# Kernel optimization log

Measured on AMD Instinct MI355X. Metric: run time of the kernel, lower is better.

Reference implementation:

```python
import jax, jax.numpy as jnp
import numpy as np

B, H, I = 4096, 128, 128


def setup_inputs() -> dict:
    key = jax.random.key(0)
    ks = jax.random.split(key, 9)
    # xavier_uniform for W1/W2: fan_in = 2H*2I, fan_out = H*2I (torch treats dim0 as fan_out for >2D differently,
    # but we only need a plausible init; exact init values don't affect correctness of the math)
    def xavier(k, shape):
        fan_in = shape[1] * shape[2] if len(shape) == 3 else shape[0]
        fan_out = shape[0] * shape[2] if len(shape) == 3 else shape[1]
        lim = np.sqrt(6.0 / (fan_in + fan_out))
        return jax.random.uniform(k, shape, jnp.float32, -lim, lim)
    W1 = xavier(ks[0], (H, 2 * H, 2 * I))
    W2 = xavier(ks[1], (H, 2 * H, 2 * I))
    W3 = xavier(ks[2], (2 * H, H))
    fan_in, fan_out = 2 * H * 2 * I, H * 2 * I
    lim = float(np.sqrt(3.0 / (0.5 * (fan_in + fan_out))))
    b1 = jax.random.uniform(ks[3], (H,), jnp.float32, -lim, lim)
    b2 = jax.random.uniform(ks[4], (H,), jnp.float32, -lim, lim)
    in0 = jax.random.normal(ks[5], (B, I), jnp.float32)
    in1 = jax.random.normal(ks[6], (B, I), jnp.float32)
    st0 = jax.random.normal(ks[7], (B, H), jnp.float32)
    st1 = jax.random.normal(ks[8], (B, H), jnp.float32)
    return {"in0": in0, "in1": in1, "st0": st0, "st1": st1,
            "W1": W1, "b1": b1, "W2": W2, "b2": b2, "W3": W3}


def reference(in0, in1, st0, st1, W1, b1, W2, b2, W3):
    s = jnp.concatenate([st0, st1], axis=1)  # [B, 2H]
    x = jnp.concatenate([in0, in1], axis=1)  # [B, 2I]
    # Trilinear contraction; same math as outer-product-then-contract:
    # einsum('ij,ik->ijk') then ('ijk,ljk->il')  ==  'bj,bk,ljk->bl'
    m1 = jnp.einsum('bj,bk,ljk->bl', s, x, W1)  # [B, H]
    m2 = jnp.einsum('bj,bk,ljk->bl', s, x, W2)  # [B, H]
    u = jax.nn.sigmoid(m2 + b2)
    state_tilda = jnp.tanh(m1 + b1)
    new_state = u * state_tilda + (1.0 - u) * (s @ W3)
    return new_state
```

## Files before the change

kernel.cpp:

```cpp
#include <hip/hip_runtime.h>
#include <hip/hip_bf16.h>
#include <stdint.h>


typedef short bf8 __attribute__((ext_vector_type(8)));
typedef float f32x4 __attribute__((ext_vector_type(4)));

static constexpr size_t WT_OFF  = 0;
static constexpr size_t XBF_OFF = 33554432 + 2097152;
static constexpr size_t MP_OFF  = XBF_OFF + 2097152;

__device__ __forceinline__ unsigned f2bf(float f) {
    unsigned u = __builtin_bit_cast(unsigned, f);
    return (u + 0x7fffu + ((u >> 16) & 1u)) >> 16;
}
__device__ __forceinline__ unsigned pack2bf(float a, float b) {
    return f2bf(a) | (f2bf(b) << 16);
}

__global__ void prep_w(const float* __restrict__ W1, const float* __restrict__ W2,
                       unsigned* __restrict__ Wt) {
    unsigned u = blockIdx.x * 256 + threadIdx.x;
    size_t e = (size_t)u * 8;
    unsigned n = (unsigned)(e >> 16);
    unsigned k = (unsigned)(e & 65535u);
    const float* src = (n < 128 ? W1 + ((size_t)n << 16)
                                : W2 + ((size_t)(n - 128) << 16)) + k;
    float4 a = ((const float4*)src)[0];
    float4 b = ((const float4*)src)[1];
    uint4 o;
    o.x = pack2bf(a.x, a.y); o.y = pack2bf(a.z, a.w);
    o.z = pack2bf(b.x, b.y); o.w = pack2bf(b.z, b.w);
    ((uint4*)Wt)[u] = o;
}

__global__ void prep_x(const float* __restrict__ in0, const float* __restrict__ in1,
                       unsigned* __restrict__ x_bf) {
    unsigned v = blockIdx.x * 256 + threadIdx.x;
    unsigned b = v >> 6;
    unsigned j4 = (v & 63u) * 4u;
    const float* src = (j4 < 128) ? (in0 + (size_t)b * 128 + j4)
                                  : (in1 + (size_t)b * 128 + (j4 - 128));
    float4 a = *(const float4*)src;
    uint2 o;
    o.x = pack2bf(a.x, a.y);
    o.y = pack2bf(a.z, a.w);
    ((uint2*)x_bf)[v] = o;
}

__launch_bounds__(256, 2)
__global__ void gemm_p(const __hip_bfloat16* __restrict__ Wt,
                       const float* __restrict__ st0, const float* __restrict__ st1,
                       const __hip_bfloat16* __restrict__ x_bf,
                       float* __restrict__ Mpart) {
    const int bx = blockIdx.x;
    const int mt = bx & 31;
    const int nt = (bx >> 5) & 1;
    const int ks = bx >> 6;
    const int b0 = mt << 7, n0 = nt << 7;
    const int tid  = threadIdx.x;
    const int lane = tid & 63, wave = tid >> 6;
    const int l15 = lane & 15, l4 = lane >> 4;

    __shared__ __align__(16) unsigned char Wl[16384];
    __shared__ __align__(16) float Sl[32 * 132];

    for (int idx = tid; idx < 4096; idx += 256) {
        int r = idx >> 5, j = idx & 31;
        int jg = ks * 32 + j;
        float v = (jg < 128) ? st0[(size_t)(b0 + r) * 128 + jg]
                             : st1[(size_t)(b0 + r) * 128 + (jg - 128)];
        Sl[j * 132 + r] = v;
    }

    const __hip_bfloat16* wgp[4];
    unsigned char* wlp[4];
    #pragma unroll
    for (int i = 0; i < 4; ++i) {
        int slot = (wave * 4 + i) * 64 + lane;
        int r = slot >> 3;
        int g = (slot & 7) ^ (r & 7);
        wgp[i] = Wt + (((size_t)(n0 + r)) << 16) + g * 8;
        wlp[i] = Wl + (wave * 4 + i) * 1024;
    }

    const unsigned char* pB = Wl + (wave * 32 + l15) * 128;
    const int be = lane & 7;
    const float* sB = Sl + l4 * 4;

    f32x4 racc[8][2];
    #pragma unroll
    for (int mf = 0; mf < 8; ++mf)
        #pragma unroll
        for (int nf = 0; nf < 2; ++nf)
            racc[mf][nf] = (f32x4){0.f, 0.f, 0.f, 0.f};

    const f32x4 zacc = (f32x4){0.f, 0.f, 0.f, 0.f};

    __syncthreads();

    for (int q = 0; q < 4; ++q) {
        bf8 a[8][2];
        const __hip_bfloat16* xb = x_bf + q * 64 + l4 * 8;
        #pragma unroll
        for (int mf = 0; mf < 8; ++mf)
            #pragma unroll
            for (int kst = 0; kst < 2; ++kst)
                a[mf][kst] = *(const bf8*)(xb + (size_t)(b0 + mf * 16 + l15) * 256 + kst * 32);

        for (int j = 0; j < 32; ++j) {
            const int koff = (ks * 32 + j) * 256 + q * 64;
            #pragma unroll
            for (int i = 0; i < 4; ++i) {
                __builtin_amdgcn_global_load_lds(
                    (__attribute__((address_space(1))) const unsigned*)(const void*)(wgp[i] + koff),
                    (__attribute__((address_space(3))) unsigned*)(void*)wlp[i],
                    16, 0, 0);
            }
            __syncthreads();

            f32x4 sv[8];
            #pragma unroll
            for (int mf = 0; mf < 8; ++mf)
                sv[mf] = *(const f32x4*)(sB + j * 132 + mf * 16);

            #pragma unroll
            for (int nf = 0; nf < 2; ++nf) {
                const unsigned char* pBn = pB + nf * 2048;
                bf8 bf0 = *(const bf8*)(pBn + ((0 + l4) ^ be) * 16);
                bf8 bf1 = *(const bf8*)(pBn + ((4 + l4) ^ be) * 16);
                #pragma unroll
                for (int mf = 0; mf < 8; ++mf) {
                    f32x4 m0 = __builtin_amdgcn_mfma_f32_16x16x32_bf16(a[mf][0], bf0, zacc, 0, 0, 0);
                    m0 = __builtin_amdgcn_mfma_f32_16x16x32_bf16(a[mf][1], bf1, m0, 0, 0, 0);
                    racc[mf][nf] += sv[mf] * m0;
                }
            }
            __syncthreads();
        }
    }

    float* mp = Mpart + ((size_t)ks << 20);
    #pragma unroll
    for (int mf = 0; mf < 8; ++mf)
        #pragma unroll
        for (int nf = 0; nf < 2; ++nf) {
            int b = b0 + mf * 16 + l4 * 4;
            int n = n0 + wave * 32 + nf * 16 + l15;
            #pragma unroll
            for (int r = 0; r < 4; ++r)
                mp[(size_t)(b + r) * 256 + n] = racc[mf][nf][r];
        }
}

__global__ void epilogue(const float* __restrict__ st0, const float* __restrict__ st1,
                         const float* __restrict__ b1, const float* __restrict__ b2,
                         const float* __restrict__ W3, const float* __restrict__ Mpart,
                         float* __restrict__ out) {
    const int tid = threadIdx.x;
    const int h = tid & 127, rg = tid >> 7;
    const int bbase = blockIdx.x * 8;
    __shared__ float srow[8][256];
    #pragma unroll
    for (int i = 0; i < 8; ++i) {
        int idx = i * 256 + tid;
        int r = idx >> 8, j = idx & 255;
        float v = (j < 128) ? st0[(size_t)(bbase + r) * 128 + j]
                            : st1[(size_t)(bbase + r) * 128 + (j - 128)];
        srow[r][j] = v;
    }
    __syncthreads();
    float acc0 = 0.f, acc1 = 0.f, acc2 = 0.f, acc3 = 0.f;
    for (int j = 0; j < 256; ++j) {
        float w = W3[j * 128 + h];
        acc0 += srow[rg][j] * w;
        acc1 += srow[rg + 2][j] * w;
        acc2 += srow[rg + 4][j] * w;
        acc3 += srow[rg + 6][j] * w;
    }
    float accs[4] = {acc0, acc1, acc2, acc3};
    float bb1 = b1[h], bb2 = b2[h];
    #pragma unroll
    for (int i = 0; i < 4; ++i) {
        int b = bbase + rg + i * 2;
        float m1 = 0.f, m2 = 0.f;
        #pragma unroll
        for (int k = 0; k < 8; ++k) {
            m1 += Mpart[((size_t)k << 20) + (size_t)b * 256 + h];
            m2 += Mpart[((size_t)k << 20) + (size_t)b * 256 + 128 + h];
        }
        float u = 1.0f / (1.0f + expf(-(m2 + bb2)));
        float t = tanhf(m1 + bb1);
        out[(size_t)b * 128 + h] = u * t + (1.0f - u) * accs[i];
    }
}

extern "C" void kernel_launch(void* const* d_in, const int* in_sizes, int n_in,
                              void* d_out, int out_size, void* d_ws, size_t ws_size,
                              hipStream_t stream) {
    const float* in0 = (const float*)d_in[0];
    const float* in1 = (const float*)d_in[1];
    const float* st0 = (const float*)d_in[2];
    const float* st1 = (const float*)d_in[3];
    const float* W1  = (const float*)d_in[4];
    const float* b1  = (const float*)d_in[5];
    const float* W2  = (const float*)d_in[6];
    const float* b2  = (const float*)d_in[7];
    const float* W3  = (const float*)d_in[8];
    float* out = (float*)d_out;
    char* ws = (char*)d_ws;

    __hip_bfloat16* Wt   = (__hip_bfloat16*)(ws + WT_OFF);
    unsigned*       x_bf = (unsigned*)(ws + XBF_OFF);
    float*          Mp   = (float*)(ws + MP_OFF);

    prep_w<<<8192, 256, 0, stream>>>(W1, W2, (unsigned*)Wt);
    prep_x<<<1024, 256, 0, stream>>>(in0, in1, x_bf);
    gemm_p<<<512, 256, 0, stream>>>(Wt, st0, st1, (const __hip_bfloat16*)x_bf, Mp);
    epilogue<<<512, 256, 0, stream>>>(st0, st1, b1, b2, W3, Mp, out);
}
```

Baseline: 294.1 us.

## Load weights directly to registers with double buffering, fuse prep kernels, remap blocks

Replaces the LDS staging of bf16 weight tiles (global_load_lds plus two barriers per step) with per-lane direct global loads into registers, double-buffered one step ahead. The K-split index becomes the fastest-varying block index, so blocks sharing weight slices run concurrently and share L2. The two prep kernels are merged into one launch, and partial-sum stores become nontemporal. Each wave now loads its own weight fragments uncoalesced from global memory and holds more registers live, which may lower occupancy.

```diff
diff --git a/kernel.cpp b/kernel.cpp
--- a/kernel.cpp
+++ b/kernel.cpp
@@ -18,34 +18,35 @@
     return f2bf(a) | (f2bf(b) << 16);
 }
 
-__global__ void prep_w(const float* __restrict__ W1, const float* __restrict__ W2,
-                       unsigned* __restrict__ Wt) {
-    unsigned u = blockIdx.x * 256 + threadIdx.x;
-    size_t e = (size_t)u * 8;
-    unsigned n = (unsigned)(e >> 16);
-    unsigned k = (unsigned)(e & 65535u);
-    const float* src = (n < 128 ? W1 + ((size_t)n << 16)
-                                : W2 + ((size_t)(n - 128) << 16)) + k;
-    float4 a = ((const float4*)src)[0];
-    float4 b = ((const float4*)src)[1];
-    uint4 o;
-    o.x = pack2bf(a.x, a.y); o.y = pack2bf(a.z, a.w);
-    o.z = pack2bf(b.x, b.y); o.w = pack2bf(b.z, b.w);
-    ((uint4*)Wt)[u] = o;
-}
-
-__global__ void prep_x(const float* __restrict__ in0, const float* __restrict__ in1,
-                       unsigned* __restrict__ x_bf) {
-    unsigned v = blockIdx.x * 256 + threadIdx.x;
-    unsigned b = v >> 6;
-    unsigned j4 = (v & 63u) * 4u;
-    const float* src = (j4 < 128) ? (in0 + (size_t)b * 128 + j4)
-                                  : (in1 + (size_t)b * 128 + (j4 - 128));
-    float4 a = *(const float4*)src;
-    uint2 o;
-    o.x = pack2bf(a.x, a.y);
-    o.y = pack2bf(a.z, a.w);
-    ((uint2*)x_bf)[v] = o;
+__global__ void prep_wx(const float* __restrict__ W1, const float* __restrict__ W2,
+                        const float* __restrict__ in0, const float* __restrict__ in1,
+                        unsigned* __restrict__ Wt, unsigned* __restrict__ x_bf) {
+    int bx = blockIdx.x;
+    if (bx < 8192) {
+        unsigned u = bx * 256 + threadIdx.x;
+        size_t e = (size_t)u * 8;
+        unsigned n = (unsigned)(e >> 16);
+        unsigned k = (unsigned)(e & 65535u);
+        const float* src = (n < 128 ? W1 + ((size_t)n << 16)
+                                    : W2 + ((size_t)(n - 128) << 16)) + k;
+        float4 a = ((const float4*)src)[0];
+        float4 b = ((const float4*)src)[1];
+        uint4 o;
+        o.x = pack2bf(a.x, a.y); o.y = pack2bf(a.z, a.w);
+        o.z = pack2bf(b.x, b.y); o.w = pack2bf(b.z, b.w);
+        ((uint4*)Wt)[u] = o;
+    } else {
+        unsigned v = (bx - 8192) * 256 + threadIdx.x;
+        unsigned b = v >> 6;
+        unsigned j4 = (v & 63u) * 4u;
+        const float* src = (j4 < 128) ? (in0 + (size_t)b * 128 + j4)
+                                      : (in1 + (size_t)b * 128 + (j4 - 128));
+        float4 a = *(const float4*)src;
+        uint2 o;
+        o.x = pack2bf(a.x, a.y);
+        o.y = pack2bf(a.z, a.w);
+        ((uint2*)x_bf)[v] = o;
+    }
 }
 
 __launch_bounds__(256, 2)
@@ -54,17 +55,15 @@
                        const __hip_bfloat16* __restrict__ x_bf,
                        float* __restrict__ Mpart) {
     const int bx = blockIdx.x;
-    const int mt = bx & 31;
-    const int nt = (bx >> 5) & 1;
-    const int ks = bx >> 6;
+    const int ks = bx & 7;
+    const int nt = (bx >> 3) & 1;
+    const int mt = bx >> 4;
     const int b0 = mt << 7, n0 = nt << 7;
     const int tid  = threadIdx.x;
     const int lane = tid & 63, wave = tid >> 6;
     const int l15 = lane & 15, l4 = lane >> 4;
 
-    __shared__ __align__(16) unsigned char Wl[16384];
     __shared__ __align__(16) float Sl[32 * 132];
-
     for (int idx = tid; idx < 4096; idx += 256) {
         int r = idx >> 5, j = idx & 31;
         int jg = ks * 32 + j;
@@ -72,20 +71,9 @@
                              : st1[(size_t)(b0 + r) * 128 + (jg - 128)];
         Sl[j * 132 + r] = v;
     }
-
-    const __hip_bfloat16* wgp[4];
-    unsigned char* wlp[4];
-    #pragma unroll
-    for (int i = 0; i < 4; ++i) {
-        int slot = (wave * 4 + i) * 64 + lane;
-        int r = slot >> 3;
-        int g = (slot & 7) ^ (r & 7);
-        wgp[i] = Wt + (((size_t)(n0 + r)) << 16) + g * 8;
-        wlp[i] = Wl + (wave * 4 + i) * 1024;
-    }
-
-    const unsigned char* pB = Wl + (wave * 32 + l15) * 128;
-    const int be = lane & 7;
+    __syncthreads();
+
+    const __hip_bfloat16* rb = Wt + ((size_t)(n0 + wave * 32 + l15) << 16) + l4 * 8;
     const float* sB = Sl + l4 * 4;
 
     f32x4 racc[8][2];
@@ -94,49 +82,54 @@
         #pragma unroll
         for (int nf = 0; nf < 2; ++nf)
             racc[mf][nf] = (f32x4){0.f, 0.f, 0.f, 0.f};
-
     const f32x4 zacc = (f32x4){0.f, 0.f, 0.f, 0.f};
 
-    __syncthreads();
-
-    for (int q = 0; q < 4; ++q) {
-        bf8 a[8][2];
-        const __hip_bfloat16* xb = x_bf + q * 64 + l4 * 8;
+    auto jkof = [&](int c) { return (ks * 32 + (c & 31)) * 256 + (c >> 5) * 64; };
+
+    bf8 buf[2][2][2];
+    #pragma unroll
+    for (int nf = 0; nf < 2; ++nf)
+        #pragma unroll
+        for (int kst = 0; kst < 2; ++kst)
+            buf[0][nf][kst] = *(const bf8*)(rb + ((size_t)nf << 20) + jkof(0) + kst * 32);
+
+    bf8 a[8][2];
+
+    #pragma unroll 2
+    for (int c = 0; c < 128; ++c) {
+        const int pp = c & 1;
+        const int q = c >> 5, j = c & 31;
+        if (j == 0) {
+            const __hip_bfloat16* xb = x_bf + q * 64 + l4 * 8;
+            #pragma unroll
+            for (int mf = 0; mf < 8; ++mf)
+                #pragma unroll
+                for (int kst = 0; kst < 2; ++kst)
+                    a[mf][kst] = *(const bf8*)(xb + (size_t)(b0 + mf * 16 + l15) * 256 + kst * 32);
+        }
+        {
+            const int c1 = (c + 1) & 127;
+            const int jk1 = jkof(c1);
+            #pragma unroll
+            for (int nf = 0; nf < 2; ++nf)
+                #pragma unroll
+                for (int kst = 0; kst < 2; ++kst)
+                    buf[pp ^ 1][nf][kst] = *(const bf8*)(rb + ((size_t)nf << 20) + jk1 + kst * 32);
+        }
+        f32x4 sv[8];
         #pragma unroll
         for (int mf = 0; mf < 8; ++mf)
-            #pragma unroll
-            for (int kst = 0; kst < 2; ++kst)
-                a[mf][kst] = *(const bf8*)(xb + (size_t)(b0 + mf * 16 + l15) * 256 + kst * 32);
-
-        for (int j = 0; j < 32; ++j) {
-            const int koff = (ks * 32 + j) * 256 + q * 64;
-            #pragma unroll
-            for (int i = 0; i < 4; ++i) {
-                __builtin_amdgcn_global_load_lds(
-                    (__attribute__((address_space(1))) const unsigned*)(const void*)(wgp[i] + koff),
-                    (__attribute__((address_space(3))) unsigned*)(void*)wlp[i],
-                    16, 0, 0);
+            sv[mf] = *(const f32x4*)(sB + j * 132 + mf * 16);
+        #pragma unroll
+        for (int nf = 0; nf < 2; ++nf) {
+            bf8 bf0 = buf[pp][nf][0];
+            bf8 bf1 = buf[pp][nf][1];
+            #pragma unroll
+            for (int mf = 0; mf < 8; ++mf) {
+                f32x4 m0 = __builtin_amdgcn_mfma_f32_16x16x32_bf16(a[mf][0], bf0, zacc, 0, 0, 0);
+                m0 = __builtin_amdgcn_mfma_f32_16x16x32_bf16(a[mf][1], bf1, m0, 0, 0, 0);
+                racc[mf][nf] += sv[mf] * m0;
             }
-            __syncthreads();
-
-            f32x4 sv[8];
-            #pragma unroll
-            for (int mf = 0; mf < 8; ++mf)
-                sv[mf] = *(const f32x4*)(sB + j * 132 + mf * 16);
-
-            #pragma unroll
-            for (int nf = 0; nf < 2; ++nf) {
-                const unsigned char* pBn = pB + nf * 2048;
-                bf8 bf0 = *(const bf8*)(pBn + ((0 + l4) ^ be) * 16);
-                bf8 bf1 = *(const bf8*)(pBn + ((4 + l4) ^ be) * 16);
-                #pragma unroll
-                for (int mf = 0; mf < 8; ++mf) {
-                    f32x4 m0 = __builtin_amdgcn_mfma_f32_16x16x32_bf16(a[mf][0], bf0, zacc, 0, 0, 0);
-                    m0 = __builtin_amdgcn_mfma_f32_16x16x32_bf16(a[mf][1], bf1, m0, 0, 0, 0);
-                    racc[mf][nf] += sv[mf] * m0;
-                }
-            }
-            __syncthreads();
         }
     }
 
@@ -149,7 +142,8 @@
             int n = n0 + wave * 32 + nf * 16 + l15;
             #pragma unroll
             for (int r = 0; r < 4; ++r)
-                mp[(size_t)(b + r) * 256 + n] = racc[mf][nf][r];
+                __builtin_nontemporal_store(racc[mf][nf][r],
+                                            &mp[(size_t)(b + r) * 256 + n]);
         }
 }
 
@@ -214,8 +208,7 @@
     unsigned*       x_bf = (unsigned*)(ws + XBF_OFF);
     float*          Mp   = (float*)(ws + MP_OFF);
 
-    prep_w<<<8192, 256, 0, stream>>>(W1, W2, (unsigned*)Wt);
-    prep_x<<<1024, 256, 0, stream>>>(in0, in1, x_bf);
+    prep_wx<<<9216, 256, 0, stream>>>(W1, W2, in0, in1, (unsigned*)Wt, x_bf);
     gemm_p<<<512, 256, 0, stream>>>(Wt, st0, st1, (const __hip_bfloat16*)x_bf, Mp);
     epilogue<<<512, 256, 0, stream>>>(st0, st1, b1, b2, W3, Mp, out);
 }
```

After: 276.0 us. 6.2% less time.
